# Performance work log

Hardware: AMD Instinct MI355X
Metric: run time of the kernel (lower is better)

The kernel has to match this reference:

```python
import jax, jax.numpy as jnp
import numpy as np

LN_EPS = 1e-5


def _gather(x, idx):
    # x: [B, N, C], idx: [B, N, K] -> [B, N, K, C]
    return jax.vmap(lambda xb, ib: xb[ib])(x, idx)


def setup_inputs() -> dict:
    key = jax.random.key(0)
    ks = jax.random.split(key, 8)
    B, N, K, C_in, C_out, GEO = 2, 16384, 32, 128, 128, 10
    return {
        "points": jax.random.normal(ks[0], (B, N, 3), dtype=jnp.float32),
        "features": jax.random.normal(ks[1], (B, N, C_in), dtype=jnp.float32),
        "grouped_idx": jax.random.randint(ks[2], (B, N, K), 0, N, dtype=jnp.int32),
        "w_pos": jax.random.normal(ks[3], (GEO, C_in), dtype=jnp.float32) * (GEO ** -0.5),
        "b_pos": jnp.zeros((C_in,), jnp.float32),
        "w_gcm": jax.random.normal(ks[4], (C_in, C_in), dtype=jnp.float32) * (C_in ** -0.5),
        "b_gcm": jnp.zeros((C_in,), jnp.float32),
        "w_out": jax.random.normal(ks[5], (C_in, C_out), dtype=jnp.float32) * (C_in ** -0.5),
        "b_out": jnp.zeros((C_out,), jnp.float32),
        "ln_g": jnp.ones((C_out,), jnp.float32),
        "ln_b": jnp.zeros((C_out,), jnp.float32),
    }


def reference(points, features, grouped_idx, w_pos, b_pos, w_gcm, b_gcm,
              w_out, b_out, ln_g, ln_b):
    # gather neighbor coords and features: [B, N, K, *]
    grouped_pts = _gather(points, grouped_idx)
    xyz = points[..., 0:3]                      # [B, N, 3]
    grouped_xyz = grouped_pts[..., 0:3]         # [B, N, K, 3]
    center = xyz[:, :, None, :]                 # [B, N, 1, 3]
    diff = grouped_xyz - center                 # xi - xj
    dist = jnp.linalg.norm(diff, axis=-1, keepdims=True)  # ||xi - xj||
    K = grouped_xyz.shape[2]
    geo = jnp.concatenate(
        [jnp.broadcast_to(center, grouped_xyz.shape), grouped_xyz, diff, dist],
        axis=-1)                                # [B, N, K, 10]
    expanded_f = geo @ w_pos + b_pos            # pos_proj -> [B, N, K, C_in]
    grouped_f = _gather(features, grouped_idx)  # [B, N, K, C_in]
    h = jax.nn.relu((grouped_f + expanded_f) @ w_gcm + b_gcm)  # gcm_layer
    pooled = jnp.max(h, axis=2)                 # maxpooling over neighbors
    res = pooled + features                     # residual
    o = res @ w_out + b_out                     # out Linear
    mu = jnp.mean(o, axis=-1, keepdims=True)
    var = jnp.mean((o - mu) ** 2, axis=-1, keepdims=True)
    o = (o - mu) * jax.lax.rsqrt(var + LN_EPS) * ln_g + ln_b  # LayerNorm
    return jax.nn.relu(o)
```

## Files before the change

kernel.cpp:

```cpp
#include <hip/hip_runtime.h>
#include <hip/hip_bf16.h>
#include <math.h>

typedef __attribute__((ext_vector_type(8))) short short8;
typedef __attribute__((ext_vector_type(4))) short short4v;
typedef __attribute__((ext_vector_type(4))) float float4v;
typedef __attribute__((ext_vector_type(2))) unsigned int uint2v;
typedef unsigned short ushort_t;

constexpr int NPTS = 32768;
constexpr int NN   = 16384;
constexpr int KK   = 32;
constexpr int CC   = 128;
constexpr int GRP  = 16;
constexpr int SR   = 136;
constexpr int SG2  = 24;
#define LN_EPS 1e-5f
#define MFMA   __builtin_amdgcn_mfma_f32_16x16x32_bf16
#define GLL(src, dst, sz) __builtin_amdgcn_global_load_lds( \
    (const __attribute__((address_space(1))) void*)(src),   \
    (__attribute__((address_space(3))) void*)(dst), sz, 0, 0)

constexpr size_t WS_FW  = 0;
constexpr size_t WS_WO  = (size_t)NPTS * CC * 2;
constexpr size_t WS_BE  = WS_WO + 32768;
constexpr size_t WS_W4  = WS_BE + 512;
constexpr size_t WS_WC  = WS_W4 + 2048;
constexpr size_t WS_WPF = WS_WC + 1536;
constexpr size_t WS_NEED = WS_WPF + 32768;
constexpr size_t FB_WP = 0, FB_WO = 40960, FB_BE = 73728, FB_PG = 74240;

__device__ __forceinline__ short f2bs(float x) {
    return (short)__builtin_bit_cast(unsigned short, __float2bfloat16(x));
}
__device__ __forceinline__ float bs2f(ushort_t u) {
    return __uint_as_float(((unsigned)u) << 16);
}

__global__ __launch_bounds__(256) void prep_w(
    const float* __restrict__ w_gcm, const float* __restrict__ w_out,
    const float* __restrict__ w_pos, const float* __restrict__ b_pos,
    const float* __restrict__ b_gcm,
    short* __restrict__ wsWpF, short* __restrict__ wsWo,
    float* __restrict__ wsBeff, short* __restrict__ wsW4, float* __restrict__ wsWc)
{
    const int t = threadIdx.x, blk = blockIdx.x;
    __shared__ float sPG[10 * 128];
    if (blk == 0) {
        #pragma unroll 4
        for (int e = t; e < 16 * 128 * 8; e += 256) {
            const int j = e & 7, n = (e >> 3) & 127, g = e >> 10;
            wsWpF[e] = f2bs(w_gcm[(g * 8 + j) * 128 + n]);
        }
    } else if (blk == 1) {
        #pragma unroll 4
        for (int e = t; e < 128 * 128; e += 256) {
            const int j = e & 7, n = (e >> 3) & 127, g = e >> 10;
            wsWo[e] = f2bs(w_out[(g * 8 + j) * 128 + n]);
        }
    } else {
        if (t < 128) {
            const int c = t;
            for (int g = 0; g < 10; ++g) {
                float s = 0.f;
                for (int r = 0; r < 128; ++r) s += w_pos[g * 128 + r] * w_gcm[r * 128 + c];
                sPG[g * 128 + c] = s;
            }
            float sb = b_gcm[c];
            for (int r = 0; r < 128; ++r) sb += b_pos[r] * w_gcm[r * 128 + c];
            wsBeff[c] = sb;
        }
        __syncthreads();
        if (t < 128) {
            const int c = t;
            short8 v = (short8)0;
            v[0] = f2bs(sPG[3 * 128 + c] + sPG[6 * 128 + c]);
            v[1] = f2bs(sPG[4 * 128 + c] + sPG[7 * 128 + c]);
            v[2] = f2bs(sPG[5 * 128 + c] + sPG[8 * 128 + c]);
            v[3] = f2bs(sPG[9 * 128 + c]);
            *(short8*)&wsW4[c * 8] = v;
            wsWc[0 * 128 + c] = sPG[0 * 128 + c] - sPG[6 * 128 + c];
            wsWc[1 * 128 + c] = sPG[1 * 128 + c] - sPG[7 * 128 + c];
            wsWc[2 * 128 + c] = sPG[2 * 128 + c] - sPG[8 * 128 + c];
        }
    }
}

__global__ __launch_bounds__(256) void prep_fw(
    const float* __restrict__ features, const short* __restrict__ wsWpF,
    ushort_t* __restrict__ wsFW)
{
    const int t = threadIdx.x, blk = blockIdx.x;
    __shared__ short sF[16 * SR];
    const int g0 = blk * GRP;
    {
        const int row = t >> 4, c8 = (t & 15) * 8;
        const float* fp = features + (size_t)(g0 + row) * CC + c8;
        const float4 a = *(const float4*)fp;
        const float4 b = *(const float4*)(fp + 4);
        short8 v;
        v[0]=f2bs(a.x); v[1]=f2bs(a.y); v[2]=f2bs(a.z); v[3]=f2bs(a.w);
        v[4]=f2bs(b.x); v[5]=f2bs(b.y); v[6]=f2bs(b.z); v[7]=f2bs(b.w);
        *(short8*)&sF[row * SR + c8] = v;
    }
    const int wv = t >> 6, lane = t & 63, quad = (lane >> 4) & 3, m = lane & 15;
    const int col0 = wv * 32 + m;
    short8 bf[4][2];
    #pragma unroll
    for (int ks = 0; ks < 4; ++ks) {
        bf[ks][0] = *((const short8*)wsWpF + ((ks * 4 + quad) * 128 + col0));
        bf[ks][1] = *((const short8*)wsWpF + ((ks * 4 + quad) * 128 + col0 + 16));
    }
    __syncthreads();
    float4v acc[2] = {};
    #pragma unroll
    for (int ks = 0; ks < 4; ++ks) {
        const short8 a = *(const short8*)(sF + m * SR + ks * 32 + quad * 8);
        acc[0] = MFMA(a, bf[ks][0], acc[0], 0, 0, 0);
        acc[1] = MFMA(a, bf[ks][1], acc[1], 0, 0, 0);
    }
    #pragma unroll
    for (int r = 0; r < 4; ++r) {
        const int R = quad * 4 + r;
        wsFW[(size_t)(g0 + R) * CC + col0]      = (ushort_t)f2bs(acc[0][r]);
        wsFW[(size_t)(g0 + R) * CC + col0 + 16] = (ushort_t)f2bs(acc[1][r]);
    }
}

__global__ __launch_bounds__(256, 3) void bridge_fw(
    const float* __restrict__ points, const float* __restrict__ features,
    const int*   __restrict__ gidx,
    const short* __restrict__ wsWo, const float* __restrict__ wsBeff,
    const short* __restrict__ wsW4, const float* __restrict__ wsWc,
    const ushort_t* __restrict__ wsFW,
    const float* __restrict__ b_out, const float* __restrict__ ln_g,
    const float* __restrict__ ln_b, float* __restrict__ out)
{
    __shared__ short sA[4][3][1024];
    __shared__ float sGxyz[GRP * KK * 3];
    __shared__ short sRes[GRP * SR];
    __shared__ short sResF[GRP * CC];
    __shared__ int   sIdx[GRP * KK];
    __shared__ float sCtr[GRP * 3];
    __shared__ float sPS[4][GRP], sPQ[4][GRP];

    const int t = threadIdx.x, wv = t >> 6, lane = t & 63;
    const int q = (lane >> 4) & 3, m = lane & 15;
    const int g0 = blockIdx.x * GRP;
    const int nbase = (g0 >= NN) ? NN : 0;
    const int colA = wv * 32 + m;
    const int rbL = lane >> 3, jL = (lane & 7) >> 1, hL = lane & 1;

    {
        const int gA = gidx[(size_t)g0 * KK + t];
        const int gB = gidx[(size_t)g0 * KK + t + 256];
        sIdx[t] = gA; sIdx[t + 256] = gB;
        const float* pA = points + (size_t)(nbase + gA) * 3;
        const float* pB = points + (size_t)(nbase + gB) * 3;
        sGxyz[t * 3 + 0] = pA[0]; sGxyz[t * 3 + 1] = pA[1]; sGxyz[t * 3 + 2] = pA[2];
        sGxyz[(t + 256) * 3 + 0] = pB[0];
        sGxyz[(t + 256) * 3 + 1] = pB[1];
        sGxyz[(t + 256) * 3 + 2] = pB[2];
    }
    if (t < GRP * 3) sCtr[t] = points[(size_t)g0 * 3 + t];
    {
        const int row = t >> 4, c8 = (t & 15) * 8;
        const float* fp = features + (size_t)(g0 + row) * CC + c8;
        const float4 a = *(const float4*)fp;
        const float4 b = *(const float4*)(fp + 4);
        short8 v;
        v[0]=f2bs(a.x); v[1]=f2bs(a.y); v[2]=f2bs(a.z); v[3]=f2bs(a.w);
        v[4]=f2bs(b.x); v[5]=f2bs(b.y); v[6]=f2bs(b.z); v[7]=f2bs(b.w);
        *(short8*)&sResF[row * CC + c8] = v;
    }

    const float beffv[2] = { wsBeff[colA], wsBeff[colA + 16] };
    float wc[6];
    #pragma unroll
    for (int i = 0; i < 3; ++i) { wc[i] = wsWc[i * 128 + colA]; wc[3 + i] = wsWc[i * 128 + colA + 16]; }
    short8 w4f[2];
    #pragma unroll
    for (int n = 0; n < 2; ++n) {
        const short8 w = *((const short8*)wsW4 + (colA + n * 16));
        w4f[n] = (q == 0) ? w : (short8)0;
    }
    const unsigned trBase = (unsigned)(size_t)(__attribute__((address_space(3))) short*)&sA[wv][0][0]
                          + (unsigned)(lane * 8);

    __syncthreads();

    auto issue_fw = [&](int p, int buf) {
        const int kw = nbase + sIdx[p * KK + rbL * 4 + jL];
        const ushort_t* s0 = wsFW + (size_t)kw * CC + wv * 32 + hL * 8;
        GLL(s0,      &sA[wv][buf][0],   16);
        GLL(s0 + 16, &sA[wv][buf][512], 16);
    };

    issue_fw(0, 0);
    issue_fw(1, 1);

    #pragma unroll
    for (int p = 0; p < GRP; ++p) {
        const int buf = p % 3;
        if (p + 2 < GRP) issue_fw(p + 2, (p + 2) % 3);
        if (p + 2 < GRP)      asm volatile("s_waitcnt vmcnt(4)" ::: "memory");
        else if (p + 1 < GRP) asm volatile("s_waitcnt vmcnt(2)" ::: "memory");
        else                  asm volatile("s_waitcnt vmcnt(0)" ::: "memory");
        __builtin_amdgcn_sched_barrier(0);

        uint2v t00, t10, t01, t11;
        const unsigned trA = trBase + (unsigned)(buf * 2048);
        asm volatile("ds_read_b64_tr_b16 %0, %1 offset:0"    : "=&v"(t00) : "v"(trA));
        asm volatile("ds_read_b64_tr_b16 %0, %1 offset:512"  : "=&v"(t10) : "v"(trA));
        asm volatile("ds_read_b64_tr_b16 %0, %1 offset:1024" : "=&v"(t01) : "v"(trA));
        asm volatile("ds_read_b64_tr_b16 %0, %1 offset:1536" : "=&v"(t11) : "v"(trA));

        const float pcx = sCtr[p * 3], pcy = sCtr[p * 3 + 1], pcz = sCtr[p * 3 + 2];
        short8 ga0 = (short8)0, ga1 = (short8)0;
        if (q == 0) {
            const int i0 = (p * KK + m) * 3, i1 = i0 + 48;
            const float ax = sGxyz[i0], ay = sGxyz[i0 + 1], az = sGxyz[i0 + 2];
            const float bx = sGxyz[i1], by = sGxyz[i1 + 1], bz = sGxyz[i1 + 2];
            const float d0x = ax - pcx, d0y = ay - pcy, d0z = az - pcz;
            const float d1x = bx - pcx, d1y = by - pcy, d1z = bz - pcz;
            const float s0 = sqrtf(d0x * d0x + d0y * d0y + d0z * d0z);
            const float s1 = sqrtf(d1x * d1x + d1y * d1y + d1z * d1z);
            ga0[0]=f2bs(ax); ga0[1]=f2bs(ay); ga0[2]=f2bs(az); ga0[3]=f2bs(s0);
            ga1[0]=f2bs(bx); ga1[1]=f2bs(by); ga1[2]=f2bs(bz); ga1[3]=f2bs(s1);
        }

        asm volatile("s_waitcnt lgkmcnt(0)" ::: "memory");
        __builtin_amdgcn_sched_barrier(0);

        float4v c00, c10, c01, c11;
        c00[0]=__uint_as_float(t00[0] << 16); c00[1]=__uint_as_float(t00[0] & 0xffff0000u);
        c00[2]=__uint_as_float(t00[1] << 16); c00[3]=__uint_as_float(t00[1] & 0xffff0000u);
        c10[0]=__uint_as_float(t10[0] << 16); c10[1]=__uint_as_float(t10[0] & 0xffff0000u);
        c10[2]=__uint_as_float(t10[1] << 16); c10[3]=__uint_as_float(t10[1] & 0xffff0000u);
        c01[0]=__uint_as_float(t01[0] << 16); c01[1]=__uint_as_float(t01[0] & 0xffff0000u);
        c01[2]=__uint_as_float(t01[1] << 16); c01[3]=__uint_as_float(t01[1] & 0xffff0000u);
        c11[0]=__uint_as_float(t11[0] << 16); c11[1]=__uint_as_float(t11[0] & 0xffff0000u);
        c11[2]=__uint_as_float(t11[1] << 16); c11[3]=__uint_as_float(t11[1] & 0xffff0000u);

        c00 = MFMA(ga0, w4f[0], c00, 0, 0, 0);
        c01 = MFMA(ga0, w4f[1], c01, 0, 0, 0);
        c10 = MFMA(ga1, w4f[0], c10, 0, 0, 0);
        c11 = MFMA(ga1, w4f[1], c11, 0, 0, 0);

        const float cb0 = pcx * wc[0] + pcy * wc[1] + pcz * wc[2];
        const float cb1 = pcx * wc[3] + pcy * wc[4] + pcz * wc[5];

        float v0 = fmaxf(fmaxf(fmaxf(c00[0],c00[1]), fmaxf(c00[2],c00[3])),
                         fmaxf(fmaxf(c10[0],c10[1]), fmaxf(c10[2],c10[3])));
        float v1 = fmaxf(fmaxf(fmaxf(c01[0],c01[1]), fmaxf(c01[2],c01[3])),
                         fmaxf(fmaxf(c11[0],c11[1]), fmaxf(c11[2],c11[3])));
        v0 = fmaxf(v0, __shfl_xor(v0, 16)); v0 = fmaxf(v0, __shfl_xor(v0, 32));
        v1 = fmaxf(v1, __shfl_xor(v1, 16)); v1 = fmaxf(v1, __shfl_xor(v1, 32));
        v0 = fmaxf(v0 + beffv[0] + cb0, 0.f);
        v1 = fmaxf(v1 + beffv[1] + cb1, 0.f);
        if (q == 0) {
            sRes[p * SR + colA]      = f2bs(v0 + bs2f((ushort_t)sResF[p * CC + colA]));
            sRes[p * SR + colA + 16] = f2bs(v1 + bs2f((ushort_t)sResF[p * CC + colA + 16]));
        }
    }

    __syncthreads();

    short8 bWo[4][2];
    #pragma unroll
    for (int ks = 0; ks < 4; ++ks)
        #pragma unroll
        for (int ntl = 0; ntl < 2; ++ntl)
            bWo[ks][ntl] = *((const short8*)wsWo + ((ks * 4 + q) * 128 + colA + ntl * 16));

    const short* rm = sRes + m * SR;
    float4v acc2[2] = {};
    #pragma unroll
    for (int ks = 0; ks < 4; ++ks) {
        const short8 a = *(const short8*)(rm + ks * 32 + q * 8);
        acc2[0] = MFMA(a, bWo[ks][0], acc2[0], 0, 0, 0);
        acc2[1] = MFMA(a, bWo[ks][1], acc2[1], 0, 0, 0);
    }

    const float boutv[2] = { b_out[colA], b_out[colA + 16] };
    const float lngv[2]  = { ln_g[colA], ln_g[colA + 16] };
    const float lnbv[2]  = { ln_b[colA], ln_b[colA + 16] };

    #pragma unroll
    for (int r = 0; r < 4; ++r) {
        const float o0 = acc2[0][r] + boutv[0];
        const float o1 = acc2[1][r] + boutv[1];
        float ss = o0 + o1, qq = o0 * o0 + o1 * o1;
        #pragma unroll
        for (int d = 1; d < 16; d <<= 1) { ss += __shfl_xor(ss, d); qq += __shfl_xor(qq, d); }
        if (m == 0) { sPS[wv][q * 4 + r] = ss; sPQ[wv][q * 4 + r] = qq; }
    }
    __syncthreads();

    #pragma unroll
    for (int r = 0; r < 4; ++r) {
        const int R = q * 4 + r;
        const float S = sPS[0][R] + sPS[1][R] + sPS[2][R] + sPS[3][R];
        const float Q = sPQ[0][R] + sPQ[1][R] + sPQ[2][R] + sPQ[3][R];
        const float mu  = S * (1.f / 128.f);
        const float var = fmaxf(Q * (1.f / 128.f) - mu * mu, 0.f);
        const float rstd = rsqrtf(var + LN_EPS);
        const float o0 = acc2[0][r] + boutv[0];
        const float o1 = acc2[1][r] + boutv[1];
        const size_t base = (size_t)(g0 + R) * CC;
        out[base + colA]      = fmaxf((o0 - mu) * rstd * lngv[0] + lnbv[0], 0.f);
        out[base + colA + 16] = fmaxf((o1 - mu) * rstd * lngv[1] + lnbv[1], 0.f);
    }
}

__global__ __launch_bounds__(128) void prep_fold_fb(
    const float* __restrict__ w_pos, const float* __restrict__ b_pos,
    const float* __restrict__ w_gcm, const float* __restrict__ b_gcm,
    float* __restrict__ wsPG, float* __restrict__ wsBeff)
{
    const int c = threadIdx.x, g = blockIdx.x;
    if (g < 10) {
        float s = 0.f;
        for (int r = 0; r < 128; ++r) s += w_pos[g * 128 + r] * w_gcm[r * 128 + c];
        wsPG[g * 128 + c] = s;
    } else {
        float s = b_gcm[c];
        for (int r = 0; r < 128; ++r) s += b_pos[r] * w_gcm[r * 128 + c];
        wsBeff[c] = s;
    }
}

__global__ __launch_bounds__(256) void prep_pack_fb(
    const float* __restrict__ w_gcm, const float* __restrict__ w_out,
    const float* __restrict__ wsPG, short* __restrict__ wsWp, short* __restrict__ wsWo)
{
    const int t = threadIdx.x, blk = blockIdx.x;
    if (blk == 0) {
        #pragma unroll 4
        for (int e = t; e < 16 * 128 * 8; e += 256) {
            const int j = e & 7, n = (e >> 3) & 127, g = e >> 10;
            wsWp[e] = f2bs(w_gcm[(g * 8 + j) * 128 + n]);
        }
    } else if (blk == 1) {
        #pragma unroll 4
        for (int e2 = t; e2 < 4 * 128 * 8; e2 += 256) {
            const int e = 16 * 128 * 8 + e2;
            const int j = e & 7, n = (e >> 3) & 127, g = e >> 10;
            const int k = g * 8 + j;
            wsWp[e] = (k < 138) ? f2bs(wsPG[(k - 128) * 128 + n]) : (short)0;
        }
    } else {
        #pragma unroll 4
        for (int e = t; e < 128 * 128; e += 256) {
            const int j = e & 7, n = (e >> 3) & 127, g = e >> 10;
            wsWo[e] = f2bs(w_out[(g * 8 + j) * 128 + n]);
        }
    }
}

__global__ __launch_bounds__(256, 3) void bridge_fb(
    const float* __restrict__ points, const float* __restrict__ features,
    const int*   __restrict__ gidx,
    const short* __restrict__ wsWp, const short* __restrict__ wsWo,
    const float* __restrict__ wsBeff,
    const float* __restrict__ b_out, const float* __restrict__ ln_g,
    const float* __restrict__ ln_b, float* __restrict__ out)
{
    __shared__ short sA[4][KK * CC];
    __shared__ short sG[3][KK * SG2];
    __shared__ short sRes[GRP * SR];
    __shared__ short sResF[GRP * CC];
    __shared__ int   sIdx[GRP * KK];
    __shared__ float sCtr[GRP * 3];
    __shared__ float sPS[4][GRP], sPQ[4][GRP];

    const int t = threadIdx.x, wv = t >> 6, lane = t & 63;
    const int quad = (lane >> 4) & 3, m = lane & 15;
    const int g0 = blockIdx.x * GRP;
    const int nbase = (g0 >= NN) ? NN : 0;
    const int col0 = wv * 32 + m;

    sIdx[t]       = gidx[(size_t)g0 * KK + t];
    sIdx[t + 256] = gidx[(size_t)g0 * KK + t + 256];
    if (t < GRP * 3) sCtr[t] = points[(size_t)g0 * 3 + t];
    {
        const float* fs = features + (size_t)g0 * CC + t * 8;
        short8 v;
        #pragma unroll
        for (int i = 0; i < 8; ++i) v[i] = f2bs(fs[i]);
        *(short8*)&sResF[t * 8] = v;
    }

    short8 bWp[5][2];
    #pragma unroll
    for (int ks = 0; ks < 5; ++ks)
        #pragma unroll
        for (int ntl = 0; ntl < 2; ++ntl)
            bWp[ks][ntl] = *((const short8*)wsWp + ((ks * 4 + quad) * 128 + col0 + ntl * 16));
    const float beffv[2] = { wsBeff[col0], wsBeff[col0 + 16] };

    __syncthreads();

    const int r0 = wv * 4 + (lane >> 4);
    const int pc = lane & 15;
    const int gc = pc ^ r0;

    float geoS[3][3];

    auto geo_load = [&](int qq) {
        if (lane < 8) {
            const int j = wv * 8 + lane;
            const int kng = nbase + sIdx[qq * KK + j];
            const float* pp = points + (size_t)kng * 3;
            const int s = qq % 3;
            geoS[s][0] = pp[0]; geoS[s][1] = pp[1]; geoS[s][2] = pp[2];
        }
    };
    auto stage = [&](int qq) {
        const int buf = qq & 3;
        const int kn0 = nbase + sIdx[qq * KK + r0];
        const int kn1 = nbase + sIdx[qq * KK + r0 + 16];
        const float4* f0 = (const float4*)(features + (size_t)kn0 * CC + gc * 8);
        const float4* f1 = (const float4*)(features + (size_t)kn1 * CC + gc * 8);
        const float4 a = f0[0], b = f0[1], c = f1[0], d = f1[1];
        short8 v;
        v[0]=f2bs(a.x); v[1]=f2bs(a.y); v[2]=f2bs(a.z); v[3]=f2bs(a.w);
        v[4]=f2bs(b.x); v[5]=f2bs(b.y); v[6]=f2bs(b.z); v[7]=f2bs(b.w);
        *(short8*)&sA[buf][r0 * CC + pc * 8] = v;
        v[0]=f2bs(c.x); v[1]=f2bs(c.y); v[2]=f2bs(c.z); v[3]=f2bs(c.w);
        v[4]=f2bs(d.x); v[5]=f2bs(d.y); v[6]=f2bs(d.z); v[7]=f2bs(d.w);
        *(short8*)&sA[buf][(r0 + 16) * CC + pc * 8] = v;
    };
    auto geo_store = [&](int qq) {
        if (lane < 8) {
            const int j = wv * 8 + lane, s = qq % 3, b = qq % 3;
            const float cx = sCtr[qq * 3], cy = sCtr[qq * 3 + 1], cz = sCtr[qq * 3 + 2];
            const float gx = geoS[s][0], gy = geoS[s][1], gz = geoS[s][2];
            const float dx = gx - cx, dy = gy - cy, dz = gz - cz;
            const float dist = sqrtf(dx * dx + dy * dy + dz * dz);
            short8 v0, v1 = (short8)0;
            v0[0]=f2bs(cx); v0[1]=f2bs(cy); v0[2]=f2bs(cz);
            v0[3]=f2bs(gx); v0[4]=f2bs(gy); v0[5]=f2bs(gz);
            v0[6]=f2bs(dx); v0[7]=f2bs(dy);
            v1[0]=f2bs(dz); v1[1]=f2bs(dist);
            *(short8*)&sG[b][j * SG2 + 0] = v0;
            *(short8*)&sG[b][j * SG2 + 8] = v1;
        }
    };

    int offA[4];
    #pragma unroll
    for (int ks = 0; ks < 4; ++ks) offA[ks] = m * CC + (((ks * 4 + quad) ^ m) * 8);
    const int offG = m * SG2 + quad * 8;

    geo_load(0); stage(0);
    geo_load(1); stage(1);
    geo_load(2); stage(2);
    geo_store(0); geo_store(1);
    __syncthreads();

    #pragma unroll
    for (int p = 0; p < GRP; ++p) {
        if (p > 0) {
            asm volatile("s_waitcnt lgkmcnt(0)" ::: "memory");
            __builtin_amdgcn_s_barrier();
        }
        __builtin_amdgcn_sched_barrier(0);
        if (p + 3 < GRP) { geo_load(p + 3); stage(p + 3); }

        const short* ab = sA[p & 3];
        const short* ag = sG[p % 3];
        float4v acc[2][2] = {};
        #pragma unroll
        for (int ks = 0; ks < 4; ++ks) {
            const short8 a0 = *(const short8*)(ab + offA[ks]);
            const short8 a1 = *(const short8*)(ab + offA[ks] + 16 * CC);
            acc[0][0] = MFMA(a0, bWp[ks][0], acc[0][0], 0, 0, 0);
            acc[0][1] = MFMA(a0, bWp[ks][1], acc[0][1], 0, 0, 0);
            acc[1][0] = MFMA(a1, bWp[ks][0], acc[1][0], 0, 0, 0);
            acc[1][1] = MFMA(a1, bWp[ks][1], acc[1][1], 0, 0, 0);
        }
        short8 ga0 = (short8)0, ga1 = (short8)0;
        if (quad < 2) {
            ga0 = *(const short8*)(ag + offG);
            ga1 = *(const short8*)(ag + offG + 16 * SG2);
        }
        acc[0][0] = MFMA(ga0, bWp[4][0], acc[0][0], 0, 0, 0);
        acc[0][1] = MFMA(ga0, bWp[4][1], acc[0][1], 0, 0, 0);
        acc[1][0] = MFMA(ga1, bWp[4][0], acc[1][0], 0, 0, 0);
        acc[1][1] = MFMA(ga1, bWp[4][1], acc[1][1], 0, 0, 0);

        #pragma unroll
        for (int ntl = 0; ntl < 2; ++ntl) {
            float v = acc[0][ntl][0];
            #pragma unroll
            for (int rr = 1; rr < 4; ++rr) v = fmaxf(v, acc[0][ntl][rr]);
            #pragma unroll
            for (int rr = 0; rr < 4; ++rr) v = fmaxf(v, acc[1][ntl][rr]);
            v = fmaxf(v, __shfl_xor(v, 16));
            v = fmaxf(v, __shfl_xor(v, 32));
            v = fmaxf(v + beffv[ntl], 0.f);
            if (quad == 0) {
                const float fc = bs2f((ushort_t)sResF[p * CC + col0 + ntl * 16]);
                sRes[p * SR + col0 + ntl * 16] = f2bs(v + fc);
            }
        }
        if (p + 2 < GRP) geo_store(p + 2);
    }

    __syncthreads();

    short8 bWo[4][2];
    #pragma unroll
    for (int ks = 0; ks < 4; ++ks)
        #pragma unroll
        for (int ntl = 0; ntl < 2; ++ntl)
            bWo[ks][ntl] = *((const short8*)wsWo + ((ks * 4 + quad) * 128 + col0 + ntl * 16));

    const short* rm = sRes + m * SR;
    float4v acc2[2] = {};
    #pragma unroll
    for (int ks = 0; ks < 4; ++ks) {
        const short8 a = *(const short8*)(rm + ks * 32 + quad * 8);
        acc2[0] = MFMA(a, bWo[ks][0], acc2[0], 0, 0, 0);
        acc2[1] = MFMA(a, bWo[ks][1], acc2[1], 0, 0, 0);
    }
    const float boutv[2] = { b_out[col0], b_out[col0 + 16] };
    const float lngv[2]  = { ln_g[col0], ln_g[col0 + 16] };
    const float lnbv[2]  = { ln_b[col0], ln_b[col0 + 16] };
    #pragma unroll
    for (int r = 0; r < 4; ++r) {
        const float o0 = acc2[0][r] + boutv[0];
        const float o1 = acc2[1][r] + boutv[1];
        float ss = o0 + o1, qq2 = o0 * o0 + o1 * o1;
        #pragma unroll
        for (int d = 1; d < 16; d <<= 1) { ss += __shfl_xor(ss, d); qq2 += __shfl_xor(qq2, d); }
        if (m == 0) { sPS[wv][quad * 4 + r] = ss; sPQ[wv][quad * 4 + r] = qq2; }
    }
    __syncthreads();
    #pragma unroll
    for (int r = 0; r < 4; ++r) {
        const int R = quad * 4 + r;
        const float S = sPS[0][R] + sPS[1][R] + sPS[2][R] + sPS[3][R];
        const float Q = sPQ[0][R] + sPQ[1][R] + sPQ[2][R] + sPQ[3][R];
        const float mu  = S * (1.f / 128.f);
        const float var = fmaxf(Q * (1.f / 128.f) - mu * mu, 0.f);
        const float rstd = rsqrtf(var + LN_EPS);
        const float o0 = acc2[0][r] + boutv[0];
        const float o1 = acc2[1][r] + boutv[1];
        const size_t base = (size_t)(g0 + R) * CC;
        out[base + col0]      = fmaxf((o0 - mu) * rstd * lngv[0] + lnbv[0], 0.f);
        out[base + col0 + 16] = fmaxf((o1 - mu) * rstd * lngv[1] + lnbv[1], 0.f);
    }
}

extern "C" void kernel_launch(void* const* d_in, const int* in_sizes, int n_in,
                              void* d_out, int out_size, void* d_ws, size_t ws_size,
                              hipStream_t stream) {
    const float* points   = (const float*)d_in[0];
    const float* features = (const float*)d_in[1];
    const int*   gidx     = (const int*)  d_in[2];
    const float* w_pos    = (const float*)d_in[3];
    const float* b_pos    = (const float*)d_in[4];
    const float* w_gcm    = (const float*)d_in[5];
    const float* b_gcm    = (const float*)d_in[6];
    const float* w_out    = (const float*)d_in[7];
    const float* b_out    = (const float*)d_in[8];
    const float* ln_g     = (const float*)d_in[9];
    const float* ln_b     = (const float*)d_in[10];
    float* out = (float*)d_out;
    char* ws = (char*)d_ws;

    if (ws_size >= WS_NEED) {
        ushort_t* wsFW   = (ushort_t*)(ws + WS_FW);
        short*    wsWo   = (short*)(ws + WS_WO);
        float*    wsBeff = (float*)(ws + WS_BE);
        short*    wsW4   = (short*)(ws + WS_W4);
        float*    wsWc   = (float*)(ws + WS_WC);
        short*    wsWpF  = (short*)(ws + WS_WPF);
        hipLaunchKernelGGL(prep_w, dim3(3), dim3(256), 0, stream,
                           w_gcm, w_out, w_pos, b_pos, b_gcm,
                           wsWpF, wsWo, wsBeff, wsW4, wsWc);
        hipLaunchKernelGGL(prep_fw, dim3(NPTS / GRP), dim3(256), 0, stream,
                           features, wsWpF, wsFW);
        hipLaunchKernelGGL(bridge_fw, dim3(NPTS / GRP), dim3(256), 0, stream,
                           points, features, gidx, wsWo, wsBeff, wsW4, wsWc, wsFW,
                           b_out, ln_g, ln_b, out);
    } else {
        short* wsWp   = (short*)(ws + FB_WP);
        short* wsWo   = (short*)(ws + FB_WO);
        float* wsBeff = (float*)(ws + FB_BE);
        float* wsPG   = (float*)(ws + FB_PG);
        hipLaunchKernelGGL(prep_fold_fb, dim3(11), dim3(128), 0, stream,
                           w_pos, b_pos, w_gcm, b_gcm, wsPG, wsBeff);
        hipLaunchKernelGGL(prep_pack_fb, dim3(3), dim3(256), 0, stream,
                           w_gcm, w_out, wsPG, wsWp, wsWo);
        hipLaunchKernelGGL(bridge_fb, dim3(NPTS / GRP), dim3(256), 0, stream,
                           points, features, gidx, wsWp, wsWo, wsBeff,
                           b_out, ln_g, ln_b, out);
    }
}
```

Baseline: 169.2 us.

## Parallelize weight folding across blocks and deepen gather prefetch to four buffers

The single-block serial fold of w_pos·w_gcm is spread over ten blocks, one per geometry row, with a separate block for the effective bias. The final packing of the folded weights into bf16 MFMA operands and centre coefficients moves into the main kernel's prologue, where each thread reads the raw folded rows. The feature gather pipeline goes from triple to quadruple buffering with a prefetch distance of three and matching vmcnt waits. The goal is to cut the serial prep-kernel latency and hide gather latency better. The cost is more LDS per block (an extra 8 KB), which may lower occupancy under the 3-blocks launch bound, plus a few extra global loads per thread in the prologue.

```diff
diff --git a/kernel.cpp b/kernel.cpp
--- a/kernel.cpp
+++ b/kernel.cpp
@@ -24,10 +24,9 @@
 constexpr size_t WS_FW  = 0;
 constexpr size_t WS_WO  = (size_t)NPTS * CC * 2;
 constexpr size_t WS_BE  = WS_WO + 32768;
-constexpr size_t WS_W4  = WS_BE + 512;
-constexpr size_t WS_WC  = WS_W4 + 2048;
-constexpr size_t WS_WPF = WS_WC + 1536;
-constexpr size_t WS_NEED = WS_WPF + 32768;
+constexpr size_t WS_WPF = WS_BE + 512;
+constexpr size_t WS_PG  = WS_WPF + 32768;
+constexpr size_t WS_NEED = WS_PG + 5120;
 constexpr size_t FB_WP = 0, FB_WO = 40960, FB_BE = 73728, FB_PG = 74240;
 
 __device__ __forceinline__ short f2bs(float x) {
@@ -37,15 +36,14 @@
     return __uint_as_float(((unsigned)u) << 16);
 }
 
-__global__ __launch_bounds__(256) void prep_w(
+__global__ __launch_bounds__(256) void prep1(
     const float* __restrict__ w_gcm, const float* __restrict__ w_out,
     const float* __restrict__ w_pos, const float* __restrict__ b_pos,
     const float* __restrict__ b_gcm,
     short* __restrict__ wsWpF, short* __restrict__ wsWo,
-    float* __restrict__ wsBeff, short* __restrict__ wsW4, float* __restrict__ wsWc)
+    float* __restrict__ wsBeff, float* __restrict__ wsPG)
 {
     const int t = threadIdx.x, blk = blockIdx.x;
-    __shared__ float sPG[10 * 128];
     if (blk == 0) {
         #pragma unroll 4
         for (int e = t; e < 16 * 128 * 8; e += 256) {
@@ -58,30 +56,21 @@
             const int j = e & 7, n = (e >> 3) & 127, g = e >> 10;
             wsWo[e] = f2bs(w_out[(g * 8 + j) * 128 + n]);
         }
+    } else if (blk < 12) {
+        if (t < 128) {
+            const int g = blk - 2, c = t;
+            float s = 0.f;
+            #pragma unroll
+            for (int r = 0; r < 128; ++r) s += w_pos[g * 128 + r] * w_gcm[r * 128 + c];
+            wsPG[g * 128 + c] = s;
+        }
     } else {
         if (t < 128) {
             const int c = t;
-            for (int g = 0; g < 10; ++g) {
-                float s = 0.f;
-                for (int r = 0; r < 128; ++r) s += w_pos[g * 128 + r] * w_gcm[r * 128 + c];
-                sPG[g * 128 + c] = s;
-            }
             float sb = b_gcm[c];
+            #pragma unroll
             for (int r = 0; r < 128; ++r) sb += b_pos[r] * w_gcm[r * 128 + c];
             wsBeff[c] = sb;
-        }
-        __syncthreads();
-        if (t < 128) {
-            const int c = t;
-            short8 v = (short8)0;
-            v[0] = f2bs(sPG[3 * 128 + c] + sPG[6 * 128 + c]);
-            v[1] = f2bs(sPG[4 * 128 + c] + sPG[7 * 128 + c]);
-            v[2] = f2bs(sPG[5 * 128 + c] + sPG[8 * 128 + c]);
-            v[3] = f2bs(sPG[9 * 128 + c]);
-            *(short8*)&wsW4[c * 8] = v;
-            wsWc[0 * 128 + c] = sPG[0 * 128 + c] - sPG[6 * 128 + c];
-            wsWc[1 * 128 + c] = sPG[1 * 128 + c] - sPG[7 * 128 + c];
-            wsWc[2 * 128 + c] = sPG[2 * 128 + c] - sPG[8 * 128 + c];
         }
     }
 }
@@ -131,12 +120,11 @@
     const float* __restrict__ points, const float* __restrict__ features,
     const int*   __restrict__ gidx,
     const short* __restrict__ wsWo, const float* __restrict__ wsBeff,
-    const short* __restrict__ wsW4, const float* __restrict__ wsWc,
-    const ushort_t* __restrict__ wsFW,
+    const float* __restrict__ wsPG, const ushort_t* __restrict__ wsFW,
     const float* __restrict__ b_out, const float* __restrict__ ln_g,
     const float* __restrict__ ln_b, float* __restrict__ out)
 {
-    __shared__ short sA[4][3][1024];
+    __shared__ short sA[4][4][1024];
     __shared__ float sGxyz[GRP * KK * 3];
     __shared__ short sRes[GRP * SR];
     __shared__ short sResF[GRP * CC];
@@ -176,12 +164,17 @@
 
     const float beffv[2] = { wsBeff[colA], wsBeff[colA + 16] };
     float wc[6];
-    #pragma unroll
-    for (int i = 0; i < 3; ++i) { wc[i] = wsWc[i * 128 + colA]; wc[3 + i] = wsWc[i * 128 + colA + 16]; }
     short8 w4f[2];
     #pragma unroll
     for (int n = 0; n < 2; ++n) {
-        const short8 w = *((const short8*)wsW4 + (colA + n * 16));
+        const int c = colA + n * 16;
+        const float p0 = wsPG[0*128+c], p1 = wsPG[1*128+c], p2 = wsPG[2*128+c];
+        const float p3 = wsPG[3*128+c], p4 = wsPG[4*128+c], p5 = wsPG[5*128+c];
+        const float p6 = wsPG[6*128+c], p7 = wsPG[7*128+c], p8 = wsPG[8*128+c];
+        const float p9 = wsPG[9*128+c];
+        wc[n*3+0] = p0 - p6; wc[n*3+1] = p1 - p7; wc[n*3+2] = p2 - p8;
+        short8 w = (short8)0;
+        w[0] = f2bs(p3 + p6); w[1] = f2bs(p4 + p7); w[2] = f2bs(p5 + p8); w[3] = f2bs(p9);
         w4f[n] = (q == 0) ? w : (short8)0;
     }
     const unsigned trBase = (unsigned)(size_t)(__attribute__((address_space(3))) short*)&sA[wv][0][0]
@@ -198,12 +191,14 @@
 
     issue_fw(0, 0);
     issue_fw(1, 1);
+    issue_fw(2, 2);
 
     #pragma unroll
     for (int p = 0; p < GRP; ++p) {
-        const int buf = p % 3;
-        if (p + 2 < GRP) issue_fw(p + 2, (p + 2) % 3);
-        if (p + 2 < GRP)      asm volatile("s_waitcnt vmcnt(4)" ::: "memory");
+        const int buf = p & 3;
+        if (p + 3 < GRP) issue_fw(p + 3, (p + 3) & 3);
+        if (p + 3 < GRP)      asm volatile("s_waitcnt vmcnt(6)" ::: "memory");
+        else if (p + 2 < GRP) asm volatile("s_waitcnt vmcnt(4)" ::: "memory");
         else if (p + 1 < GRP) asm volatile("s_waitcnt vmcnt(2)" ::: "memory");
         else                  asm volatile("s_waitcnt vmcnt(0)" ::: "memory");
         __builtin_amdgcn_sched_barrier(0);
@@ -250,10 +245,10 @@
         const float cb0 = pcx * wc[0] + pcy * wc[1] + pcz * wc[2];
         const float cb1 = pcx * wc[3] + pcy * wc[4] + pcz * wc[5];
 
-        float v0 = fmaxf(fmaxf(fmaxf(c00[0],c00[1]), fmaxf(c00[2],c00[3])),
-                         fmaxf(fmaxf(c10[0],c10[1]), fmaxf(c10[2],c10[3])));
-        float v1 = fmaxf(fmaxf(fmaxf(c01[0],c01[1]), fmaxf(c01[2],c01[3])),
-                         fmaxf(fmaxf(c11[0],c11[1]), fmaxf(c11[2],c11[3])));
+        float v0 = fmaxf(fmaxf(fmaxf(c00[0], c00[1]), fmaxf(c00[2], c00[3])),
+                         fmaxf(fmaxf(c10[0], c10[1]), fmaxf(c10[2], c10[3])));
+        float v1 = fmaxf(fmaxf(fmaxf(c01[0], c01[1]), fmaxf(c01[2], c01[3])),
+                         fmaxf(fmaxf(c11[0], c11[1]), fmaxf(c11[2], c11[3])));
         v0 = fmaxf(v0, __shfl_xor(v0, 16)); v0 = fmaxf(v0, __shfl_xor(v0, 32));
         v1 = fmaxf(v1, __shfl_xor(v1, 16)); v1 = fmaxf(v1, __shfl_xor(v1, 32));
         v0 = fmaxf(v0 + beffv[0] + cb0, 0.f);
@@ -575,16 +570,15 @@
         ushort_t* wsFW   = (ushort_t*)(ws + WS_FW);
         short*    wsWo   = (short*)(ws + WS_WO);
         float*    wsBeff = (float*)(ws + WS_BE);
-        short*    wsW4   = (short*)(ws + WS_W4);
-        float*    wsWc   = (float*)(ws + WS_WC);
         short*    wsWpF  = (short*)(ws + WS_WPF);
-        hipLaunchKernelGGL(prep_w, dim3(3), dim3(256), 0, stream,
+        float*    wsPG   = (float*)(ws + WS_PG);
+        hipLaunchKernelGGL(prep1, dim3(13), dim3(256), 0, stream,
                            w_gcm, w_out, w_pos, b_pos, b_gcm,
-                           wsWpF, wsWo, wsBeff, wsW4, wsWc);
+                           wsWpF, wsWo, wsBeff, wsPG);
         hipLaunchKernelGGL(prep_fw, dim3(NPTS / GRP), dim3(256), 0, stream,
                            features, wsWpF, wsFW);
         hipLaunchKernelGGL(bridge_fw, dim3(NPTS / GRP), dim3(256), 0, stream,
-                           points, features, gidx, wsWo, wsBeff, wsW4, wsWc, wsFW,
+                           points, features, gidx, wsWo, wsBeff, wsPG, wsFW,
                            b_out, ln_g, ln_b, out);
     } else {
         short* wsWp   = (short*)(ws + FB_WP);
```

Measured after the change: 149.5 us. 1.13x faster.
